# Kernel tuning notes

Measured on AMD Instinct MI355X. Metric: run time of the kernel, lower is better.

## Reference

```python
import jax, jax.numpy as jnp
import numpy as np
from jax import lax

B, N, C, W, D = 128, 16384, 8, 10, 3   # batch, input_size, n_channels, out_window, poly_degree
L = N - W + 1                          # in-filter tap length
EPS = 1e-5


def setup_inputs() -> dict:
    key = jax.random.key(0)
    ks = jax.random.split(key, 8)
    x = jax.random.normal(ks[0], (B, N, C, 2), dtype=jnp.float32)
    # torch Linear-style scale ~ 1/sqrt(fan_in)
    w_in_real = jax.random.normal(ks[1], (C, L), dtype=jnp.float32) * (L ** -0.5)
    w_in_imag = jax.random.normal(ks[2], (C, L), dtype=jnp.float32) * (L ** -0.5)
    fan_coeff = 2 * (C - 1) * D
    w_coeff = jax.random.normal(ks[3], (C, 2, fan_coeff), dtype=jnp.float32) * (fan_coeff ** -0.5)
    w_out_real = jax.random.normal(ks[4], (C, W), dtype=jnp.float32) * (W ** -0.5)
    w_out_imag = jax.random.normal(ks[5], (C, W), dtype=jnp.float32) * (W ** -0.5)
    bn_gamma = jnp.ones((C,), dtype=jnp.float32)
    bn_beta = jnp.zeros((C,), dtype=jnp.float32)
    return {"x": x, "w_in_real": w_in_real, "w_in_imag": w_in_imag,
            "w_coeff": w_coeff, "w_out_real": w_out_real,
            "w_out_imag": w_out_imag, "bn_gamma": bn_gamma, "bn_beta": bn_beta}


# complement index map: row c lists all channels != c
_IDX = np.array([[j for j in range(C) if j != c] for c in range(C)])  # (C, C-1)


def _grouped_fir(sig, w):
    # sig: (B, N, C); per-channel length-L correlation -> (B, W, C)
    out = lax.conv_general_dilated(
        jnp.transpose(sig, (0, 2, 1)),      # (B, C, N)
        w[:, None, :],                      # (C, 1, L)
        window_strides=(1,), padding='VALID', feature_group_count=C)
    return jnp.transpose(out, (0, 2, 1))    # (B, W, C)


def reference(x, w_in_real, w_in_imag, w_coeff, w_out_real, w_out_imag, bn_gamma, bn_beta):
    fr = _grouped_fir(x[..., 0], w_in_real)   # (B, W, C)
    fi = _grouped_fir(x[..., 1], w_in_imag)   # (B, W, C)

    # polynomial expansion: pow_d = fr^d + fi^d, d = 1..D
    powd = jnp.stack([fr ** d + fi ** d for d in range(1, D + 1)], axis=-1)  # (B, W, C, D)
    poly_r = powd * fr[..., None]
    poly_i = powd * fi[..., None]

    # cross-channel coeff layers: input layout = [real(all j != c), imag(all j != c)]
    rg = poly_r[:, :, _IDX, :]                      # (B, W, C, C-1, D)
    ig = poly_i[:, :, _IDX, :]
    Wc = w_coeff.reshape(C, 2, 2, C - 1, D)         # (c, out, real/imag half, j, d)
    nonlin = (jnp.einsum('bwcjd,cpjd->bwcp', rg, Wc[:, :, 0]) +
              jnp.einsum('bwcjd,cpjd->bwcp', ig, Wc[:, :, 1]))  # (B, W, C, 2)

    out_r = jnp.einsum('bwc,cw->bc', nonlin[..., 0], w_out_real)
    out_i = jnp.einsum('bwc,cw->bc', nonlin[..., 1], w_out_imag)
    out = jnp.stack([out_r, out_i], axis=-1)        # (B, C, 2)

    # BatchNorm1d over (batch, last) per channel, training-mode batch stats
    mean = out.mean(axis=(0, 2), keepdims=True)
    var = out.var(axis=(0, 2), keepdims=True)
    return (out - mean) / jnp.sqrt(var + EPS) * bn_gamma[None, :, None] + bn_beta[None, :, None]
```

## Files before the change

kernel.cpp:

```cpp
#include <hip/hip_runtime.h>

#define BB 128
#define NN 16384
#define CC 8
#define WW 10
#define DD 3
#define LL 16375
#define LP 16392
#define SEG 8
#define CHLEN 64
#define BPB 16
#define ABLK (BB / BPB)

typedef float f2_t __attribute__((ext_vector_type(2)));

__global__ __launch_bounds__(256) void k_interleave(const float* __restrict__ wr,
                                                    const float* __restrict__ wi,
                                                    float* __restrict__ w2) {
  int idx = blockIdx.x * 256 + threadIdx.x;
  if (idx >= LP * CC) return;
  int l = idx >> 3;
  int c = idx & 7;
  float a = 0.f, b = 0.f;
  if (l < LL) { a = wr[c * LL + l]; b = wi[c * LL + l]; }
  w2[2 * idx]     = a;
  w2[2 * idx + 1] = b;
}

__global__ __launch_bounds__(256) void k_fir(const float* __restrict__ x,
                                             const float* __restrict__ w2,
                                             float* __restrict__ fpart) {
  int b   = blockIdx.x >> 3;
  int seg = blockIdx.x & 7;
  int tid = threadIdx.x;
  int c     = tid & 7;
  int chunk = tid >> 3;
  int n0 = seg * (NN / SEG) + chunk * CHLEN;

  const f2_t* __restrict__ xp  = ((const f2_t*)x)  + (size_t)b * NN * CC + c;
  const f2_t* __restrict__ wpt = ((const f2_t*)w2) + c;

  f2_t acc[WW];
#pragma unroll
  for (int w = 0; w < WW; ++w) acc[w] = (f2_t)0.f;

  f2_t prev[9];
#pragma unroll
  for (int k = 0; k < 9; ++k) {
    int l = n0 - 9 + k;
    prev[k] = (l >= 0) ? wpt[(size_t)l * CC] : (f2_t)0.f;
  }

  for (int g = 0; g < CHLEN / 16; ++g) {
    int nb = n0 + g * 16;
    f2_t wv[16], xv[16];
#pragma unroll
    for (int u = 0; u < 16; ++u) {
      wv[u] = wpt[(size_t)(nb + u) * CC];
      xv[u] = xp[(size_t)(nb + u) * CC];
    }
#pragma unroll
    for (int u = 0; u < 16; ++u) {
#pragma unroll
      for (int w = 0; w < WW; ++w) {
        int idx = u - w;
        f2_t wt = (idx >= 0) ? wv[idx] : prev[idx + 9];
        acc[w][0] += xv[u][0] * wt[0];
        acc[w][1] += xv[u][1] * wt[1];
      }
    }
#pragma unroll
    for (int k = 0; k < 9; ++k) prev[k] = wv[7 + k];
  }

  __shared__ float red[256 * 20];
#pragma unroll
  for (int w = 0; w < WW; ++w) {
    red[tid * 20 + 2 * w]     = acc[w][0];
    red[tid * 20 + 2 * w + 1] = acc[w][1];
  }
  __syncthreads();
  if (tid < 160) {
    int cc = (tid >> 1) & 7;
    int wv_ = tid >> 4;
    int ri = tid & 1;
    int k  = 2 * wv_ + ri;
    float s = 0.f;
    for (int ch = 0; ch < 32; ++ch) s += red[(ch * 8 + cc) * 20 + k];
    fpart[(size_t)blockIdx.x * 160 + tid] = s;
  }
}

__global__ __launch_bounds__(256) void k_nonlin(const float* __restrict__ fpart,
                                                const float* __restrict__ wc,
                                                const float* __restrict__ wor,
                                                const float* __restrict__ woi,
                                                float* __restrict__ oraw,
                                                float* __restrict__ part) {
  __shared__ float sred[BPB][164];
  __shared__ float swc[704];
  __shared__ float swout[160];

  int tid = threadIdx.x;
  int blk = blockIdx.x;
  int b0 = blk * BPB;

  for (int i = tid; i < 672; i += 256) swc[i] = wc[i];
  if (tid < 80) swout[tid] = wor[tid];
  else if (tid < 160) swout[tid] = woi[tid - 80];

  {
    const float4* fp4 = (const float4*)fpart;
    for (int o4 = tid; o4 < BPB * 40; o4 += 256) {
      int bl = o4 / 40;
      int r4 = o4 - bl * 40;
      float4 s = {0.f, 0.f, 0.f, 0.f};
      size_t base = ((size_t)(b0 + bl) * 8) * 40 + r4;
#pragma unroll
      for (int seg = 0; seg < 8; ++seg) {
        float4 v = fp4[base + (size_t)seg * 40];
        s.x += v.x; s.y += v.y; s.z += v.z; s.w += v.w;
      }
      int r = r4 * 4;
      sred[bl][r] = s.x; sred[bl][r + 1] = s.y; sred[bl][r + 2] = s.z; sred[bl][r + 3] = s.w;
    }
  }
  __syncthreads();

  int b = tid >> 4;
  int c = (tid >> 1) & 7;
  int p = tid & 1;

  float wreg[8][2][3];
#pragma unroll
  for (int j = 0; j < 8; ++j) {
    int jj = j - (j > c ? 1 : 0);
    if (j == c) jj = 0;
#pragma unroll
    for (int ri = 0; ri < 2; ++ri)
#pragma unroll
      for (int d = 0; d < 3; ++d) {
        float v = swc[(c * 2 + p) * 42 + ri * 21 + jj * 3 + d];
        wreg[j][ri][d] = (j == c) ? 0.f : v;
      }
  }

  float o = 0.f;
  const float* wop = swout + p * 80 + c * 10;
#pragma unroll
  for (int w = 0; w < WW; ++w) {
    float4 f0 = *(const float4*)&sred[b][w * 16];
    float4 f1 = *(const float4*)&sred[b][w * 16 + 4];
    float4 f2 = *(const float4*)&sred[b][w * 16 + 8];
    float4 f3 = *(const float4*)&sred[b][w * 16 + 12];
    float fv[16] = {f0.x, f0.y, f0.z, f0.w, f1.x, f1.y, f1.z, f1.w,
                    f2.x, f2.y, f2.z, f2.w, f3.x, f3.y, f3.z, f3.w};
    float nl0 = 0.f, nl1 = 0.f, nl2 = 0.f;
#pragma unroll
    for (int j = 0; j < 8; ++j) {
      float r  = fv[2 * j];
      float im = fv[2 * j + 1];
      float r2 = r * r, i2 = im * im;
      float pw0 = r + im;
      float pw1 = r2 + i2;
      float pw2 = r2 * r + i2 * im;
      nl0 += (pw0 * r) * wreg[j][0][0] + (pw0 * im) * wreg[j][1][0];
      nl1 += (pw1 * r) * wreg[j][0][1] + (pw1 * im) * wreg[j][1][1];
      nl2 += (pw2 * r) * wreg[j][0][2] + (pw2 * im) * wreg[j][1][2];
    }
    o += (nl0 + nl1 + nl2) * wop[w];
  }

  oraw[((size_t)(b0 + b) * CC + c) * 2 + p] = o;

  __shared__ float sval[256], ssq[256];
  sval[tid] = o;
  ssq[tid]  = o * o;
  __syncthreads();
  if (tid < 8) {
    float S = 0.f, Q = 0.f;
#pragma unroll
    for (int k = 0; k < 32; ++k) {
      int t = (k >> 1) * 16 + tid * 2 + (k & 1);
      S += sval[t];
      Q += ssq[t];
    }
    part[(blk * 8 + tid) * 2 + 0] = S;
    part[(blk * 8 + tid) * 2 + 1] = Q;
  }
}

__global__ __launch_bounds__(256) void k_bn(const float* __restrict__ oraw,
                                            const float* __restrict__ part,
                                            const float* __restrict__ gamma,
                                            const float* __restrict__ beta,
                                            float* __restrict__ out) {
  __shared__ float mv[8], iv[8], bv[8];
  int tid = threadIdx.x;
  if (tid < 8) {
    float S = 0.f, Q = 0.f;
#pragma unroll
    for (int blk = 0; blk < ABLK; ++blk) {
      S += part[(blk * 8 + tid) * 2 + 0];
      Q += part[(blk * 8 + tid) * 2 + 1];
    }
    float mean = S * (1.0f / 256.0f);
    float var  = Q * (1.0f / 256.0f) - mean * mean;
    mv[tid] = mean;
    iv[tid] = gamma[tid] * rsqrtf(var + 1e-5f);
    bv[tid] = beta[tid];
  }
  __syncthreads();
  for (int i = tid; i < BB * CC * 2; i += 256) {
    int c = (i >> 1) & 7;
    out[i] = (oraw[i] - mv[c]) * iv[c] + bv[c];
  }
}

extern "C" void kernel_launch(void* const* d_in, const int* in_sizes, int n_in,
                              void* d_out, int out_size, void* d_ws, size_t ws_size,
                              hipStream_t stream) {
  const float* x   = (const float*)d_in[0];
  const float* wr  = (const float*)d_in[1];
  const float* wi  = (const float*)d_in[2];
  const float* wc  = (const float*)d_in[3];
  const float* wor = (const float*)d_in[4];
  const float* woi = (const float*)d_in[5];
  const float* gm  = (const float*)d_in[6];
  const float* bt  = (const float*)d_in[7];
  float* out = (float*)d_out;

  float* ws    = (float*)d_ws;
  float* w2    = ws;
  float* fpart = w2 + (size_t)CC * LP * 2;
  float* oraw  = fpart + (size_t)BB * SEG * 160;
  float* part  = oraw + BB * CC * 2;

  k_interleave<<<dim3((LP * CC + 255) / 256), dim3(256), 0, stream>>>(wr, wi, w2);
  k_fir<<<dim3(BB * SEG), dim3(256), 0, stream>>>(x, w2, fpart);
  k_nonlin<<<dim3(ABLK), dim3(256), 0, stream>>>(fpart, wc, wor, woi, oraw, part);
  k_bn<<<dim3(1), dim3(256), 0, stream>>>(oraw, part, gm, bt, out);
}
```

Before: 48.58 us.

## Tile FIR over batch and N, stage weights in shared memory, drop interleave kernel

Reorganizes the FIR kernel so each block handles 8 batches across a 512-sample N tile. The block loads the interleaved real/imag filter taps for that tile into LDS once and reuses them across the 8 batches, instead of reading a pre-interleaved weight buffer from global memory per batch. This removes the separate interleave kernel launch and cuts weight traffic by a factor of the batch tile. In exchange, the number of per-tile partial sums grows from 8 to 32 per batch, which the nonlin kernel now has to reduce, and an extra barrier is added for the shared memory reuse.

```diff
diff --git a/kernel.cpp b/kernel.cpp
--- a/kernel.cpp
+++ b/kernel.cpp
@@ -4,41 +4,50 @@
 #define NN 16384
 #define CC 8
 #define WW 10
-#define DD 3
 #define LL 16375
-#define LP 16392
-#define SEG 8
-#define CHLEN 64
+#define NT 512
+#define NTILES (NN / NT)
+#define BT 8
+#define BTILES (BB / BT)
+#define WSL (NT + 9)
 #define BPB 16
 #define ABLK (BB / BPB)
 
 typedef float f2_t __attribute__((ext_vector_type(2)));
 
-__global__ __launch_bounds__(256) void k_interleave(const float* __restrict__ wr,
-                                                    const float* __restrict__ wi,
-                                                    float* __restrict__ w2) {
-  int idx = blockIdx.x * 256 + threadIdx.x;
-  if (idx >= LP * CC) return;
-  int l = idx >> 3;
-  int c = idx & 7;
-  float a = 0.f, b = 0.f;
-  if (l < LL) { a = wr[c * LL + l]; b = wi[c * LL + l]; }
-  w2[2 * idx]     = a;
-  w2[2 * idx + 1] = b;
-}
-
 __global__ __launch_bounds__(256) void k_fir(const float* __restrict__ x,
-                                             const float* __restrict__ w2,
+                                             const float* __restrict__ wr,
+                                             const float* __restrict__ wi,
                                              float* __restrict__ fpart) {
-  int b   = blockIdx.x >> 3;
-  int seg = blockIdx.x & 7;
+  __shared__ float smem[WSL * CC * 2];
+  f2_t* sw2 = (f2_t*)smem;
+
+  int nt = blockIdx.x & (NTILES - 1);
+  int bt = blockIdx.x >> 5;
   int tid = threadIdx.x;
-  int c     = tid & 7;
-  int chunk = tid >> 3;
-  int n0 = seg * (NN / SEG) + chunk * CHLEN;
-
-  const f2_t* __restrict__ xp  = ((const f2_t*)x)  + (size_t)b * NN * CC + c;
-  const f2_t* __restrict__ wpt = ((const f2_t*)w2) + c;
+  int ntile = nt * NT;
+  int l0 = ntile - 9;
+
+  {
+    int cs = tid >> 5;
+    int jj = tid & 31;
+    for (int j = jj; j < WSL; j += 32) {
+      int l = l0 + j;
+      float a = 0.f, bb = 0.f;
+      if (l >= 0 && l < LL) { a = wr[cs * LL + l]; bb = wi[cs * LL + l]; }
+      f2_t v; v[0] = a; v[1] = bb;
+      sw2[cs * WSL + j] = v;
+    }
+  }
+  __syncthreads();
+
+  int c    = tid & 7;
+  int bsub = (tid >> 3) & 7;
+  int nh   = tid >> 6;
+  int b    = bt * BT + bsub;
+
+  const f2_t* __restrict__ xp = ((const f2_t*)x) + ((size_t)b * NN + ntile + nh * 128) * CC + c;
+  const f2_t* wp = sw2 + c * WSL + nh * 128 + 9;
 
   f2_t acc[WW];
 #pragma unroll
@@ -46,18 +55,14 @@
 
   f2_t prev[9];
 #pragma unroll
-  for (int k = 0; k < 9; ++k) {
-    int l = n0 - 9 + k;
-    prev[k] = (l >= 0) ? wpt[(size_t)l * CC] : (f2_t)0.f;
-  }
-
-  for (int g = 0; g < CHLEN / 16; ++g) {
-    int nb = n0 + g * 16;
+  for (int k = 0; k < 9; ++k) prev[k] = wp[k - 9];
+
+  for (int g = 0; g < 8; ++g) {
     f2_t wv[16], xv[16];
 #pragma unroll
     for (int u = 0; u < 16; ++u) {
-      wv[u] = wpt[(size_t)(nb + u) * CC];
-      xv[u] = xp[(size_t)(nb + u) * CC];
+      wv[u] = wp[g * 16 + u];
+      xv[u] = xp[(size_t)(g * 16 + u) * CC];
     }
 #pragma unroll
     for (int u = 0; u < 16; ++u) {
@@ -73,21 +78,21 @@
     for (int k = 0; k < 9; ++k) prev[k] = wv[7 + k];
   }
 
-  __shared__ float red[256 * 20];
+  __syncthreads();
+  float* red = smem;
+  int rb = (nh * 8 + bsub) * 160 + c * 2;
 #pragma unroll
   for (int w = 0; w < WW; ++w) {
-    red[tid * 20 + 2 * w]     = acc[w][0];
-    red[tid * 20 + 2 * w + 1] = acc[w][1];
-  }
-  __syncthreads();
-  if (tid < 160) {
-    int cc = (tid >> 1) & 7;
-    int wv_ = tid >> 4;
-    int ri = tid & 1;
-    int k  = 2 * wv_ + ri;
-    float s = 0.f;
-    for (int ch = 0; ch < 32; ++ch) s += red[(ch * 8 + cc) * 20 + k];
-    fpart[(size_t)blockIdx.x * 160 + tid] = s;
+    red[rb + w * 16]     = acc[w][0];
+    red[rb + w * 16 + 1] = acc[w][1];
+  }
+  __syncthreads();
+  for (int t = tid; t < BT * 160; t += 256) {
+    int bs = t / 160;
+    int r  = t - bs * 160;
+    float s = red[(0 * 8 + bs) * 160 + r] + red[(1 * 8 + bs) * 160 + r]
+            + red[(2 * 8 + bs) * 160 + r] + red[(3 * 8 + bs) * 160 + r];
+    fpart[((size_t)(bt * BT + bs) * NTILES + nt) * 160 + r] = s;
   }
 }
 
@@ -115,9 +120,9 @@
       int bl = o4 / 40;
       int r4 = o4 - bl * 40;
       float4 s = {0.f, 0.f, 0.f, 0.f};
-      size_t base = ((size_t)(b0 + bl) * 8) * 40 + r4;
-#pragma unroll
-      for (int seg = 0; seg < 8; ++seg) {
+      size_t base = ((size_t)(b0 + bl) * NTILES) * 40 + r4;
+#pragma unroll
+      for (int seg = 0; seg < NTILES; ++seg) {
         float4 v = fp4[base + (size_t)seg * 40];
         s.x += v.x; s.y += v.y; s.z += v.z; s.w += v.w;
       }
@@ -231,13 +236,11 @@
   float* out = (float*)d_out;
 
   float* ws    = (float*)d_ws;
-  float* w2    = ws;
-  float* fpart = w2 + (size_t)CC * LP * 2;
-  float* oraw  = fpart + (size_t)BB * SEG * 160;
+  float* fpart = ws;
+  float* oraw  = fpart + (size_t)BB * NTILES * 160;
   float* part  = oraw + BB * CC * 2;
 
-  k_interleave<<<dim3((LP * CC + 255) / 256), dim3(256), 0, stream>>>(wr, wi, w2);
-  k_fir<<<dim3(BB * SEG), dim3(256), 0, stream>>>(x, w2, fpart);
+  k_fir<<<dim3(BTILES * NTILES), dim3(256), 0, stream>>>(x, wr, wi, fpart);
   k_nonlin<<<dim3(ABLK), dim3(256), 0, stream>>>(fpart, wc, wor, woi, oraw, part);
   k_bn<<<dim3(1), dim3(256), 0, stream>>>(oraw, part, gm, bt, out);
 }
```

New measurement: 46.20 us. 1.05x faster.
